# Kernel optimization log

Measured on AMD Instinct MI355X. Metric: run time of the kernel, lower is better.

Reference implementation:

```python
import jax, jax.numpy as jnp
import numpy as np

B, G, P, C = 16, 14, 16, 3          # batch, patch grid (14x14), patch size, channels
D, DI, HM, L = 384, 768, 1536, 12   # embed_dim, d_inner=expand*D, mlp_hidden=4*D, depth


def _ln(x, g, b, eps=1e-5):
    m = x.mean(-1, keepdims=True)
    v = ((x - m) ** 2).mean(-1, keepdims=True)
    return (x - m) * jax.lax.rsqrt(v + eps) * g + b


def _lin_attn(seq, wi, bi, wo, bo, g, b):
    # LinearAttention fallback: gated pointwise MLP (SiLU(z)*sigmoid(gate)) + LN + proj_out
    zg = seq @ wi + bi
    z, gate = jnp.split(zg, 2, axis=-1)
    z = jax.nn.silu(z) * jax.nn.sigmoid(gate)
    return _ln(z, g, b) @ wo + bo


def setup_inputs():
    key = jax.random.key(0)
    ks = jax.random.split(key, 8)
    def w(k, shape, s=0.02):
        return (jax.random.normal(k, shape) * s).astype(jnp.float32)
    return {
        'x': jax.random.normal(ks[0], (B, C, G * P, G * P), jnp.float32),
        'patch_w': w(ks[1], (C * P * P, D)), 'patch_b': jnp.zeros((D,), jnp.float32),
        'pe_g': jnp.ones((D,), jnp.float32), 'pe_b': jnp.zeros((D,), jnp.float32),
        'pos': w(ks[2], (1, G * G, D)),
        'n1_g': jnp.ones((L, D), jnp.float32), 'n1_b': jnp.zeros((L, D), jnp.float32),
        'pi_w': w(ks[3], (L, 4, D, 2 * DI)), 'pi_b': jnp.zeros((L, 4, 2 * DI), jnp.float32),
        'po_w': w(ks[4], (L, 4, DI, D)), 'po_b': jnp.zeros((L, 4, D), jnp.float32),
        'la_g': jnp.ones((L, 4, DI), jnp.float32), 'la_b': jnp.zeros((L, 4, DI), jnp.float32),
        'mg_w': w(ks[5], (L, 4 * D, D)), 'mg_b': jnp.zeros((L, D), jnp.float32),
        'sn_g': jnp.ones((L, D), jnp.float32), 'sn_b': jnp.zeros((L, D), jnp.float32),
        'n2_g': jnp.ones((L, D), jnp.float32), 'n2_b': jnp.zeros((L, D), jnp.float32),
        'm1_w': w(ks[6], (L, D, HM)), 'm1_b': jnp.zeros((L, HM), jnp.float32),
        'm2_w': w(ks[7], (L, HM, D)), 'm2_b': jnp.zeros((L, D), jnp.float32),
        'fin_g': jnp.ones((D,), jnp.float32), 'fin_b': jnp.zeros((D,), jnp.float32),
    }


def reference(x, patch_w, patch_b, pe_g, pe_b, pos, n1_g, n1_b, pi_w, pi_b, po_w, po_b,
              la_g, la_b, mg_w, mg_b, sn_g, sn_b, n2_g, n2_b, m1_w, m1_b, m2_w, m2_b,
              fin_g, fin_b):
    Bsz = x.shape[0]
    # Patch embed: non-overlapping conv == per-patch linear projection
    patches = x.reshape(Bsz, C, G, P, G, P).transpose(0, 2, 4, 1, 3, 5).reshape(Bsz, G, G, C * P * P)
    h = _ln(patches @ patch_w + patch_b, pe_g, pe_b)          # [B, G, G, D]
    h = (h.reshape(Bsz, G * G, D) + pos).reshape(Bsz, G, G, D)  # pos embed (no interp: grid==base)
    for l in range(L):
        hn = _ln(h, n1_g[l], n1_b[l])
        # 4-direction scan sequences (-> <- down up)
        ht = hn.transpose(0, 2, 1, 3)
        seqs = [hn.reshape(Bsz, G * G, D),
                hn[:, ::-1, ::-1].reshape(Bsz, G * G, D),
                ht.reshape(Bsz, G * G, D),
                ht[:, ::-1, ::-1].reshape(Bsz, G * G, D)]
        outs = []
        for i in range(4):
            o = _lin_attn(seqs[i], pi_w[l, i], pi_b[l, i], po_w[l, i], po_b[l, i], la_g[l, i], la_b[l, i])
            if i == 1:
                o = o[:, ::-1]
            elif i == 2:
                o = o.reshape(Bsz, G, G, D).transpose(0, 2, 1, 3).reshape(Bsz, G * G, D)
            elif i == 3:
                o = o[:, ::-1].reshape(Bsz, G, G, D).transpose(0, 2, 1, 3).reshape(Bsz, G * G, D)
            outs.append(o)
        merged = jnp.concatenate(outs, axis=-1) @ mg_w[l] + mg_b[l]
        merged = _ln(merged, sn_g[l], sn_b[l]).reshape(Bsz, G, G, D)
        h = h + merged
        hn2 = _ln(h, n2_g[l], n2_b[l])
        h = h + (jax.nn.gelu(hn2 @ m1_w[l] + m1_b[l], approximate=False) @ m2_w[l] + m2_b[l])
    return _ln(h.reshape(Bsz, G * G, D), fin_g, fin_b)  # dense features [B, N, D]
```

## Files before the change

### kernel.cpp

```cpp
#include <hip/hip_runtime.h>
#include <math.h>

typedef unsigned short u16;
typedef __bf16 bf16x8 __attribute__((ext_vector_type(8)));
typedef float f32x4 __attribute__((ext_vector_type(4)));

#define L_   12
#define NTOK 3136
#define MP   3200

__device__ __forceinline__ float b2f(u16 v){ return __builtin_bit_cast(float, (unsigned)v<<16); }
__device__ __forceinline__ u16 f2b(float f){
    unsigned u = __builtin_bit_cast(unsigned, f);
    u += 0x7fffu + ((u>>16)&1u);
    return (u16)(u>>16);
}
__device__ __forceinline__ float wsum(float v){
    #pragma unroll
    for (int o=32;o;o>>=1) v += __shfl_xor(v,o);
    return v;
}
__device__ __forceinline__ void gl_lds16(const void* g, void* l){
    __builtin_amdgcn_global_load_lds(
        (const __attribute__((address_space(1))) void*)g,
        (__attribute__((address_space(3))) void*)l, 16, 0, 0);
}

__device__ __host__ __forceinline__ int rho16(int c){
    return (c < 768) ? (((c>>4)<<5) + (c&15)) : ((((c-768)>>4)<<5) + 16 + ((c-768)&15));
}

__global__ __launch_bounds__(256) void k_transpose(const float* __restrict__ src,
                                                   u16* __restrict__ dst, int R, int C){
    __shared__ float t[32][33];
    long long base = (long long)blockIdx.z * R * C;
    int c0 = blockIdx.x<<5, r0 = blockIdx.y<<5;
    int tx = threadIdx.x & 31, ty = threadIdx.x >> 5;
    #pragma unroll
    for (int i=0;i<32;i+=8)
        t[ty+i][tx] = src[base + (long long)(r0+ty+i)*C + c0 + tx];
    __syncthreads();
    #pragma unroll
    for (int i=0;i<32;i+=8)
        dst[base + (long long)(c0+ty+i)*R + r0 + tx] = f2b(t[tx][ty+i]);
}

__global__ __launch_bounds__(256) void k_transpose_pi(const float* __restrict__ src,
                                                      u16* __restrict__ dst){
    const int R = 384, C = 1536;
    __shared__ float t[32][33];
    long long base = (long long)blockIdx.z * R * C;
    int c0 = blockIdx.x<<5, r0 = blockIdx.y<<5;
    int tx = threadIdx.x & 31, ty = threadIdx.x >> 5;
    #pragma unroll
    for (int i=0;i<32;i+=8)
        t[ty+i][tx] = src[base + (long long)(r0+ty+i)*C + c0 + tx];
    __syncthreads();
    #pragma unroll
    for (int i=0;i<32;i+=8){
        int c = c0 + ty + i;
        dst[base + (long long)rho16(c)*R + r0 + tx] = f2b(t[tx][ty+i]);
    }
}

__global__ __launch_bounds__(256) void k_bi(const float* __restrict__ pi_b, float* __restrict__ out){
    int idx = blockIdx.x*256 + threadIdx.x;
    if (idx >= 48*1536) return;
    int slab = idx / 1536, c = idx - slab*1536;
    int l = slab >> 2, dir = slab & 3;
    out[(long long)l*6144 + dir*1536 + rho16(c)] = pi_b[idx];
}

__global__ __launch_bounds__(256) void k_cvt_g(const float4* __restrict__ src,
                                               const float* __restrict__ la_g,
                                               ushort4* __restrict__ dst){
    int i = blockIdx.x*256 + threadIdx.x;
    if (i >= 3538944) return;
    int flat = i*4;
    int z = flat / 294912, rem = flat - z*294912;
    int ci = rem / 384;
    float gsc = la_g[(long long)z*768 + ci];
    float4 v = src[i];
    ushort4 o; o.x=f2b(v.x*gsc); o.y=f2b(v.y*gsc); o.z=f2b(v.z*gsc); o.w=f2b(v.w*gsc);
    dst[i] = o;
}

__global__ __launch_bounds__(384) void k_bw(const float* __restrict__ la_b,
                                            const float* __restrict__ po_w,
                                            const float* __restrict__ po_b,
                                            const float* __restrict__ mg_w,
                                            float* __restrict__ bcb){
    __shared__ float t[384];
    int z = blockIdx.x; int l = z>>2, dir = z&3;
    int i = threadIdx.x;
    const float* pw = po_w + (long long)z*294912;
    const float* lb = la_b + (long long)z*768;
    float s = 0.f;
    for (int ci=0; ci<768; ci++) s = fmaf(lb[ci], pw[(long long)ci*384 + i], s);
    t[i] = s + po_b[(long long)z*384 + i];
    __syncthreads();
    const float* mw = mg_w + (long long)l*589824 + (long long)dir*384*384;
    float o = 0.f;
    for (int m=0;m<384;m++) o = fmaf(t[m], mw[(long long)m*384 + i], o);
    bcb[(long long)z*384 + i] = o;
}

__global__ __launch_bounds__(384) void k_gsum(const u16* __restrict__ WcT, float* __restrict__ G){
    int z = blockIdx.x; int l = z>>2, dir = z&3;
    int n = threadIdx.x;
    const u16* p = WcT + (long long)l*1179648 + (long long)n*3072 + dir*768;
    float s = 0.f;
    for (int ci=0; ci<768; ci+=4){
        ushort4 v = *reinterpret_cast<const ushort4*>(p + ci);
        s += b2f(v.x)+b2f(v.y)+b2f(v.z)+b2f(v.w);
    }
    G[(long long)z*384 + n] = s;
}

__global__ __launch_bounds__(256) void k_stats(const u16* __restrict__ gated,
                                               float* __restrict__ st){
    int unit = blockIdx.x*4 + (threadIdx.x>>6);
    int lane = threadIdx.x & 63;
    const u16* p = gated + (long long)(unit>>2)*3072 + (unit&3)*768;
    float s1 = 0.f, s2 = 0.f;
    #pragma unroll
    for (int i=0;i<3;i++){
        ushort4 v = *reinterpret_cast<const ushort4*>(p + i*256 + lane*4);
        const u16* a = (const u16*)&v;
        #pragma unroll
        for (int q=0;q<4;q++){ float f = b2f(a[q]); s1 += f; s2 += f*f; }
    }
    s1 = wsum(s1); s2 = wsum(s2);
    if (lane==0){
        st[(long long)unit*2]   = s1;
        st[(long long)unit*2+1] = s2;
    }
}

__global__ __launch_bounds__(256) void k_patches(const float* __restrict__ x, u16* __restrict__ out){
    int idx = blockIdx.x*256 + threadIdx.x;
    int row = idx / 768, col = idx - row*768;
    float v = 0.f;
    if (row < NTOK){
        int b = row / 196, t = row - b*196;
        int gi = t / 14, gj = t - gi*14;
        int c = col >> 8, rem = col & 255, pi = rem >> 4, pj = rem & 15;
        v = x[((long long)(b*3 + c)*224 + gi*16 + pi)*224 + gj*16 + pj];
    }
    out[idx] = f2b(v);
}

template<int EPI, int BM>
__global__ __launch_bounds__(256) void gemm_tn(
    const u16* __restrict__ A, int lda, long long aSh, long long aSl,
    const u16* __restrict__ Bt, int ldb, long long bSh, long long bSl,
    const float* __restrict__ bias, long long biasSh, int splitBias,
    void* __restrict__ Cbase, int ldc, long long cSh, long long cSl,
    int K, int zshift, const float* __restrict__ aux)
{
    constexpr int NF = (BM==128) ? 4 : 2;
    constexpr int AI = (BM==128) ? 4 : 2;
    int z = blockIdx.z;
    int zh = z >> zshift, zl = z - (zh << zshift);
    const u16* Az  = A  + zh*aSh + zl*aSl;
    const u16* Btz = Bt + zh*bSh + zl*bSl;
    bool addb = bias && (!splitBias || zl == 0);
    long long cOff = zh*cSh + zl*cSl;
    int m0 = blockIdx.y*BM, n0 = blockIdx.x*128;

    __shared__ u16 As[2][BM*64];
    __shared__ u16 Bs[2][8192];

    int tid = threadIdx.x;
    int lane = tid & 63;
    int w = tid >> 6;
    int wrb = (BM==128) ? (w>>1)*64 : 0;
    int wcb = (BM==128) ? (w&1)*64 : w*32;
    int rsub = lane >> 3, csub = lane & 7;
    int scol = ((csub ^ rsub) << 3);
    int kxor = (lane & 7) << 4;

    const u16* ga[AI]; const u16* gb[4]; int loa[AI], lob[4];
    #pragma unroll
    for (int j=0;j<AI;j++){
        int r = j*32 + w*8 + rsub;
        ga[j] = Az + (long long)(m0 + r)*lda + scol;
        loa[j] = (j*32 + w*8)*64;
    }
    #pragma unroll
    for (int j=0;j<4;j++){
        int r = j*32 + w*8 + rsub;
        gb[j] = Btz + (long long)(n0 + r)*ldb + scol;
        lob[j] = (j*32 + w*8)*64;
    }

    f32x4 acc[4][NF];
    #pragma unroll
    for (int m=0;m<4;m++)
        #pragma unroll
        for (int n=0;n<NF;n++) acc[m][n] = (f32x4){0.f,0.f,0.f,0.f};

    int nkt = K >> 6;

    auto stage = [&](int ko, int p){
        #pragma unroll
        for (int j=0;j<AI;j++) gl_lds16(ga[j] + ko, &As[p][loa[j]]);
        #pragma unroll
        for (int j=0;j<4;j++)  gl_lds16(gb[j] + ko, &Bs[p][lob[j]]);
    };

    stage(0, 0);
    stage(64, 1);

    auto step = [&](int kt, int p){
        if (kt == nkt-1)               asm volatile("s_waitcnt vmcnt(0)" ::: "memory");
        else if constexpr (BM==128)    asm volatile("s_waitcnt vmcnt(8)" ::: "memory");
        else                           asm volatile("s_waitcnt vmcnt(6)" ::: "memory");
        __builtin_amdgcn_s_barrier();
        const char* as = (const char*)As[p];
        const char* bs = (const char*)Bs[p];
        bf16x8 af[2][4], bfr[2][NF];
        #pragma unroll
        for (int kk=0; kk<2; ++kk){
            int kb = ((kk*32 + ((lane>>4)<<3))*2) ^ kxor;
            #pragma unroll
            for (int m=0;m<4;m++){
                int r = wrb + m*16 + (lane&15);
                af[kk][m] = *reinterpret_cast<const bf16x8*>(as + r*128 + kb);
            }
            #pragma unroll
            for (int n=0;n<NF;n++){
                int r = wcb + n*16 + (lane&15);
                bfr[kk][n] = *reinterpret_cast<const bf16x8*>(bs + r*128 + kb);
            }
        }
        asm volatile("s_waitcnt lgkmcnt(0)" ::: "memory");
        __builtin_amdgcn_sched_barrier(0);
        __builtin_amdgcn_s_barrier();
        if (kt+2 < nkt) stage((kt+2)<<6, p);
        #pragma unroll
        for (int kk=0; kk<2; ++kk)
            #pragma unroll
            for (int m=0;m<4;m++)
                #pragma unroll
                for (int n=0;n<NF;n++)
                    acc[m][n] = __builtin_amdgcn_mfma_f32_16x16x32_bf16(af[kk][m], bfr[kk][n], acc[m][n], 0,0,0);
    };

    for (int kt=0; kt<nkt; kt+=2){ step(kt, 0); step(kt+1, 1); }

    int rbase = m0 + wrb;
    int nbase = n0 + wcb;
    if (EPI==3){
        int dir = n0/1536;
        #pragma unroll
        for (int np2=0; np2<NF/2; ++np2){
            int ncz = nbase + (np2*2)*16 + (lane&15);
            int pz  = ncz - dir*1536;
            int ci  = ((pz>>5)<<4) + (pz&15);
            float bz = addb ? bias[ncz]      : 0.f;
            float bg = addb ? bias[ncz+16]   : 0.f;
            #pragma unroll
            for (int m=0;m<4;m++){
                #pragma unroll
                for (int r4=0;r4<4;r4++){
                    int row = rbase + m*16 + ((lane>>4)<<2) + r4;
                    float vz = acc[m][np2*2][r4]   + bz;
                    float vg = acc[m][np2*2+1][r4] + bg;
                    float gv = vz / ((1.f+__expf(-vz))*(1.f+__expf(-vg)));
                    ((u16*)Cbase)[(long long)row*3072 + dir*768 + ci] = f2b(gv);
                }
            }
        }
    } else if (EPI==4){
        #pragma unroll
        for (int m=0;m<4;m++){
            #pragma unroll
            for (int r4=0;r4<4;r4++){
                int row = rbase + m*16 + ((lane>>4)<<2) + r4;
                float st1 = aux[((long long)row*4 + zl)*2];
                float st2 = aux[((long long)row*4 + zl)*2 + 1];
                float mu = st1*(1.f/768.f);
                float rs = rsqrtf(st2*(1.f/768.f) - mu*mu + 1e-5f);
                #pragma unroll
                for (int n=0;n<NF;n++){
                    int ncol = nbase + n*16 + (lane&15);
                    ((float*)Cbase)[(long long)row*ldc + ncol + cOff] = acc[m][n][r4]*rs;
                }
            }
        }
    } else {
        #pragma unroll
        for (int m=0;m<4;m++){
            #pragma unroll
            for (int n=0;n<NF;n++){
                int ncol = nbase + n*16 + (lane&15);
                float bv = addb ? bias[zh*biasSh + ncol] : 0.f;
                #pragma unroll
                for (int r4=0;r4<4;r4++){
                    int row = rbase + m*16 + ((lane>>4)<<2) + r4;
                    float v = acc[m][n][r4] + bv;
                    long long idx = (long long)row*ldc + ncol + cOff;
                    if (EPI==0)      ((u16*)Cbase)[idx] = f2b(v);
                    else if (EPI==1){
                        float gl = 0.5f*v*(1.f + erff(v*0.70710678118f));
                        ((u16*)Cbase)[idx] = f2b(gl);
                    }
                    else             ((float*)Cbase)[idx] = v;
                }
            }
        }
    }
}

template<int MODE>
__global__ __launch_bounds__(256) void k_addln(float* __restrict__ h,
        const float* __restrict__ parts, int np,
        const float* __restrict__ g, const float* __restrict__ b, void* __restrict__ out){
    int row = blockIdx.x*4 + (threadIdx.x>>6);
    int lane = threadIdx.x & 63;
    float* hp = h + (long long)row*384;
    float v[6]; float s = 0.f;
    #pragma unroll
    for (int i=0;i<6;i++){
        int c = lane + i*64;
        float t = hp[c];
        for (int p=0;p<np;p++) t += parts[(long long)p*MP*384 + (long long)row*384 + c];
        v[i] = t; s += t;
    }
    if (MODE==0 && np){
        #pragma unroll
        for (int i=0;i<6;i++) hp[lane + i*64] = v[i];
    }
    float mu = wsum(s)*(1.f/384.f);
    float q = 0.f;
    #pragma unroll
    for (int i=0;i<6;i++){ float d = v[i]-mu; q += d*d; }
    float rs = rsqrtf(wsum(q)*(1.f/384.f) + 1e-5f);
    if (MODE==0){
        u16* op = (u16*)out + (long long)row*384;
        #pragma unroll
        for (int i=0;i<6;i++){ int c = lane + i*64; op[c] = f2b((v[i]-mu)*rs*g[c] + b[c]); }
    } else {
        float* op = (float*)out + (long long)row*384;
        #pragma unroll
        for (int i=0;i<6;i++){ int c = lane + i*64; op[c] = (v[i]-mu)*rs*g[c] + b[c]; }
    }
}

__global__ __launch_bounds__(256) void k_pe_ln(const float* __restrict__ parts,
        const float* __restrict__ g, const float* __restrict__ b,
        const float* __restrict__ pos, float* __restrict__ h,
        const float* __restrict__ n1g, const float* __restrict__ n1b,
        u16* __restrict__ hn){
    int row = blockIdx.x*4 + (threadIdx.x>>6);
    int lane = threadIdx.x & 63;
    float v[6]; float s = 0.f;
    #pragma unroll
    for (int i=0;i<6;i++){
        int c = lane + i*64;
        float t = parts[(long long)row*384 + c] + parts[(long long)MP*384 + (long long)row*384 + c];
        v[i] = t; s += t;
    }
    float mu = wsum(s)*(1.f/384.f);
    float q = 0.f;
    #pragma unroll
    for (int i=0;i<6;i++){ float d = v[i]-mu; q += d*d; }
    float rs = rsqrtf(wsum(q)*(1.f/384.f) + 1e-5f);
    int t = row % 196;
    const float* pp = pos + (long long)t*384;
    float* op = h + (long long)row*384;
    float hv[6]; float s2 = 0.f;
    #pragma unroll
    for (int i=0;i<6;i++){
        int c = lane + i*64;
        float nv = (v[i]-mu)*rs*g[c] + b[c] + pp[c];
        op[c] = nv; hv[i] = nv; s2 += nv;
    }
    float mu2 = wsum(s2)*(1.f/384.f);
    float q2 = 0.f;
    #pragma unroll
    for (int i=0;i<6;i++){ float d = hv[i]-mu2; q2 += d*d; }
    float rs2 = rsqrtf(wsum(q2)*(1.f/384.f) + 1e-5f);
    u16* hp = hn + (long long)row*384;
    #pragma unroll
    for (int i=0;i<6;i++){ int c = lane + i*64; hp[c] = f2b((hv[i]-mu2)*rs2*n1g[c] + n1b[c]); }
}

__global__ __launch_bounds__(256) void k_sn_ln(const float* __restrict__ parts,
        const float* __restrict__ bcb, const float* __restrict__ G,
        const float* __restrict__ st, const float* __restrict__ mgb,
        const float* __restrict__ sg, const float* __restrict__ sb,
        float* __restrict__ h,
        const float* __restrict__ n2g, const float* __restrict__ n2b,
        u16* __restrict__ hn2){
    int row = blockIdx.x*4 + (threadIdx.x>>6);
    int lane = threadIdx.x & 63;
    float murs[4];
    #pragma unroll
    for (int z=0;z<4;z++){
        float st1 = st[((long long)row*4 + z)*2];
        float st2 = st[((long long)row*4 + z)*2 + 1];
        float mu = st1*(1.f/768.f);
        float rs = rsqrtf(st2*(1.f/768.f) - mu*mu + 1e-5f);
        murs[z] = mu*rs;
    }
    float v[6]; float s = 0.f;
    #pragma unroll
    for (int i=0;i<6;i++){
        int c = lane + i*64;
        long long o = (long long)row*384 + c;
        float t = mgb[c];
        #pragma unroll
        for (int z=0;z<4;z++) t += bcb[z*384+c] - murs[z]*G[z*384+c];
        #pragma unroll
        for (int p=0;p<4;p++) t += parts[(long long)p*MP*384 + o];
        v[i] = t; s += t;
    }
    float mu = wsum(s)*(1.f/384.f);
    float q = 0.f;
    #pragma unroll
    for (int i=0;i<6;i++){ float d = v[i]-mu; q += d*d; }
    float rs = rsqrtf(wsum(q)*(1.f/384.f) + 1e-5f);
    float* hp = h + (long long)row*384;
    float hv[6]; float s2 = 0.f;
    #pragma unroll
    for (int i=0;i<6;i++){
        int c = lane + i*64;
        float nv = hp[c] + (v[i]-mu)*rs*sg[c] + sb[c];
        hp[c] = nv; hv[i] = nv; s2 += nv;
    }
    float mu2 = wsum(s2)*(1.f/384.f);
    float q2 = 0.f;
    #pragma unroll
    for (int i=0;i<6;i++){ float d = hv[i]-mu2; q2 += d*d; }
    float rs2 = rsqrtf(wsum(q2)*(1.f/384.f) + 1e-5f);
    u16* op = hn2 + (long long)row*384;
    #pragma unroll
    for (int i=0;i<6;i++){ int c = lane + i*64; op[c] = f2b((hv[i]-mu2)*rs2*n2g[c] + n2b[c]); }
}

extern "C" void kernel_launch(void* const* d_in, const int* in_sizes, int n_in,
                              void* d_out, int out_size, void* d_ws, size_t ws_size,
                              hipStream_t stream)
{
    const float* x      = (const float*)d_in[0];
    const float* patch_w= (const float*)d_in[1];
    const float* patch_b= (const float*)d_in[2];
    const float* pe_g   = (const float*)d_in[3];
    const float* pe_b   = (const float*)d_in[4];
    const float* pos    = (const float*)d_in[5];
    const float* n1_g   = (const float*)d_in[6];
    const float* n1_b   = (const float*)d_in[7];
    const float* pi_w   = (const float*)d_in[8];
    const float* pi_b   = (const float*)d_in[9];
    const float* po_w   = (const float*)d_in[10];
    const float* po_b   = (const float*)d_in[11];
    const float* la_g   = (const float*)d_in[12];
    const float* la_b   = (const float*)d_in[13];
    const float* mg_w   = (const float*)d_in[14];
    const float* mg_b   = (const float*)d_in[15];
    const float* sn_g   = (const float*)d_in[16];
    const float* sn_b   = (const float*)d_in[17];
    const float* n2_g   = (const float*)d_in[18];
    const float* n2_b   = (const float*)d_in[19];
    const float* m1_w   = (const float*)d_in[20];
    const float* m1_b   = (const float*)d_in[21];
    const float* m2_w   = (const float*)d_in[22];
    const float* m2_b   = (const float*)d_in[23];
    const float* fin_g  = (const float*)d_in[24];
    const float* fin_b  = (const float*)d_in[25];

    char* wptr = (char*)d_ws;
    auto carve = [&](long long elems, int esz)->void*{
        void* p = (void*)wptr;
        wptr += ((elems*(long long)esz + 255)/256)*256;
        return p;
    };

    u16* wt_pi  = (u16*)carve(28311552, 2);
    u16* wt_mgr = (u16*)carve(7077888, 2);
    u16* wt_m1  = (u16*)carve(7077888, 2);
    u16* wt_m2  = (u16*)carve(7077888, 2);
    u16* wt_pe  = (u16*)carve(294912, 2);
    u16* po_bf  = (u16*)carve(14155776, 2);
    u16* WcT    = (u16*)carve(14155776, 2);
    float* bcb  = (float*)carve(48*384, 4);
    float* Gs   = (float*)carve(48*384, 4);
    float* stats= (float*)carve(MP*8, 4);
    float* pib_i= (float*)carve(12*6144, 4);
    float* h    = (float*)carve((long long)MP*384, 4);
    float* parts= (float*)carve(4LL*MP*384, 4);
    u16* patches= (u16*)carve((long long)MP*768, 2);
    u16* hn     = (u16*)carve((long long)MP*384, 2);
    u16* gated  = (u16*)carve((long long)MP*3072, 2);
    u16* outs   = (u16*)carve((long long)MP*1536, 2);

    dim3 blk(256);

    k_transpose_pi<<<dim3(48,12,48), blk, 0, stream>>>(pi_w, wt_pi);
    k_bi<<<dim3((48*1536+255)/256), blk, 0, stream>>>(pi_b, pib_i);
    k_transpose<<<dim3(12,12,48), blk, 0, stream>>>(mg_w,   wt_mgr, 384, 384);
    k_transpose<<<dim3(48,12,12), blk, 0, stream>>>(m1_w,   wt_m1, 384, 1536);
    k_transpose<<<dim3(12,48,12), blk, 0, stream>>>(m2_w,   wt_m2, 1536, 384);
    k_transpose<<<dim3(12,24,1),  blk, 0, stream>>>(patch_w,wt_pe, 768, 384);
    k_cvt_g<<<dim3(13824), blk, 0, stream>>>((const float4*)po_w, la_g, (ushort4*)po_bf);
    k_bw<<<dim3(48), dim3(384), 0, stream>>>(la_b, po_w, po_b, mg_w, bcb);
    gemm_tn<0,128><<<dim3(6,3,48), blk, 0, stream>>>(
        wt_mgr, 384, 589824LL, 147456LL,
        po_bf,  384, 1179648LL, 294912LL,
        nullptr, 0, 0,
        WcT, 3072, 1179648LL, 768LL, 384, 2, nullptr);
    k_gsum<<<dim3(48), dim3(384), 0, stream>>>(WcT, Gs);

    k_patches<<<dim3(MP*768/256), blk, 0, stream>>>(x, patches);
    gemm_tn<2,64><<<dim3(3,50,2), blk, 0, stream>>>(
        patches, 768, 0, 384,
        wt_pe,   768, 0, 384,
        patch_b, 0, 1,
        parts, 384, 0, (long long)MP*384, 384, 1, nullptr);
    k_pe_ln<<<dim3(MP/4), blk, 0, stream>>>(parts, pe_g, pe_b, pos, h, n1_g, n1_b, hn);

    for (int l=0; l<L_; ++l){
        gemm_tn<3,128><<<dim3(48,25,1), blk, 0, stream>>>(
            hn, 384, 0, 0,
            wt_pi + (long long)l*2359296, 384, 0, 0,
            pib_i + (long long)l*6144, 0, 0,
            gated, 3072, 0, 0, 384, 0, nullptr);
        k_stats<<<dim3(MP), blk, 0, stream>>>(gated, stats);
        gemm_tn<4,64><<<dim3(3,50,4), blk, 0, stream>>>(
            gated, 3072, 0, 768,
            WcT + (long long)l*1179648, 3072, 0, 768,
            nullptr, 0, 0,
            parts, 384, 0, (long long)MP*384, 768, 2, stats);
        k_sn_ln<<<dim3(MP/4), blk, 0, stream>>>(parts,
                                                bcb + (long long)l*1536, Gs + (long long)l*1536,
                                                stats, mg_b + l*384,
                                                sn_g + l*384, sn_b + l*384,
                                                h, n2_g + l*384, n2_b + l*384, hn);
        gemm_tn<1,64><<<dim3(12,50,1), blk, 0, stream>>>(
            hn, 384, 0, 0,
            wt_m1 + (long long)l*589824, 384, 0, 0,
            m1_b + (long long)l*1536, 0, 0,
            outs, 1536, 0, 0, 384, 0, nullptr);
        gemm_tn<2,64><<<dim3(3,50,4), blk, 0, stream>>>(
            outs, 1536, 0, 384,
            wt_m2 + (long long)l*589824, 1536, 0, 384,
            m2_b + l*384, 0, 1,
            parts, 384, 0, (long long)MP*384, 384, 2, nullptr);
        if (l < L_-1)
            k_addln<0><<<dim3(MP/4), blk, 0, stream>>>(h, parts, 4,
                n1_g + (l+1)*384, n1_b + (l+1)*384, hn);
        else
            k_addln<1><<<dim3(NTOK/4), blk, 0, stream>>>(h, parts, 4,
                fin_g, fin_b, (float*)d_out);
    }
}
```

Measured before the change: 1.395 ms.

## Fold LN mean correction into GEMM epilogue, split bias precompute, halve MLP2 split-K

Splits the serial per-slab bias kernel into two chunked kernels that accumulate with atomics, and sums the four direction biases into one vector per layer. The weight row sums come from a new GEMM epilogue instead of a separate pass. The mean*G correction moves into the merge GEMM epilogue, so the LN kernel reads less. The MLP2 GEMM split-K drops from 4 to 2 parts, cutting partial-sum traffic in the add+LN kernel at the cost of fewer blocks. Atomics need a memset and make results order-dependent.

```diff
diff --git a/kernel.cpp b/kernel.cpp
--- a/kernel.cpp
+++ b/kernel.cpp
@@ -85,36 +85,33 @@
     dst[i] = o;
 }
 
-__global__ __launch_bounds__(384) void k_bw(const float* __restrict__ la_b,
-                                            const float* __restrict__ po_w,
-                                            const float* __restrict__ po_b,
-                                            const float* __restrict__ mg_w,
-                                            float* __restrict__ bcb){
-    __shared__ float t[384];
-    int z = blockIdx.x; int l = z>>2, dir = z&3;
+__global__ __launch_bounds__(384) void k_bw1(const float* __restrict__ la_b,
+                                             const float* __restrict__ po_w,
+                                             float* __restrict__ tvec){
+    int z = blockIdx.x, chunk = blockIdx.y;
     int i = threadIdx.x;
     const float* pw = po_w + (long long)z*294912;
     const float* lb = la_b + (long long)z*768;
     float s = 0.f;
-    for (int ci=0; ci<768; ci++) s = fmaf(lb[ci], pw[(long long)ci*384 + i], s);
-    t[i] = s + po_b[(long long)z*384 + i];
-    __syncthreads();
-    const float* mw = mg_w + (long long)l*589824 + (long long)dir*384*384;
-    float o = 0.f;
-    for (int m=0;m<384;m++) o = fmaf(t[m], mw[(long long)m*384 + i], o);
-    bcb[(long long)z*384 + i] = o;
-}
-
-__global__ __launch_bounds__(384) void k_gsum(const u16* __restrict__ WcT, float* __restrict__ G){
-    int z = blockIdx.x; int l = z>>2, dir = z&3;
-    int n = threadIdx.x;
-    const u16* p = WcT + (long long)l*1179648 + (long long)n*3072 + dir*768;
+    int c0 = chunk*128;
+    for (int ci=c0; ci<c0+128; ci++) s = fmaf(lb[ci], pw[(long long)ci*384 + i], s);
+    atomicAdd(tvec + (long long)z*384 + i, s);
+}
+
+__global__ __launch_bounds__(384) void k_bw2(const float* __restrict__ tvec,
+                                             const float* __restrict__ po_b,
+                                             const float* __restrict__ mg_w,
+                                             float* __restrict__ fullb){
+    int z = blockIdx.x, chunk = blockIdx.y;
+    int l = z>>2, dir = z&3;
+    int i = threadIdx.x;
+    const float* mw = mg_w + (long long)l*589824 + (long long)dir*147456;
+    const float* tv = tvec + (long long)z*384;
+    const float* pb = po_b + (long long)z*384;
     float s = 0.f;
-    for (int ci=0; ci<768; ci+=4){
-        ushort4 v = *reinterpret_cast<const ushort4*>(p + ci);
-        s += b2f(v.x)+b2f(v.y)+b2f(v.z)+b2f(v.w);
-    }
-    G[(long long)z*384 + n] = s;
+    int m0 = chunk*64;
+    for (int m=m0; m<m0+64; m++) s = fmaf(tv[m]+pb[m], mw[(long long)m*384 + i], s);
+    atomicAdd(fullb + (long long)l*384 + i, s);
 }
 
 __global__ __launch_bounds__(256) void k_stats(const u16* __restrict__ gated,
@@ -156,7 +153,7 @@
     const u16* __restrict__ Bt, int ldb, long long bSh, long long bSl,
     const float* __restrict__ bias, long long biasSh, int splitBias,
     void* __restrict__ Cbase, int ldc, long long cSh, long long cSl,
-    int K, int zshift, const float* __restrict__ aux)
+    int K, int zshift, const float* __restrict__ aux, float* __restrict__ auxw)
 {
     constexpr int NF = (BM==128) ? 4 : 2;
     constexpr int AI = (BM==128) ? 4 : 2;
@@ -285,8 +282,28 @@
                 #pragma unroll
                 for (int n=0;n<NF;n++){
                     int ncol = nbase + n*16 + (lane&15);
-                    ((float*)Cbase)[(long long)row*ldc + ncol + cOff] = acc[m][n][r4]*rs;
+                    float gsv = bias[(long long)zl*384 + ncol];
+                    ((float*)Cbase)[(long long)row*ldc + ncol + cOff] = (acc[m][n][r4] - mu*gsv)*rs;
                 }
+            }
+        }
+    } else if (EPI==5){
+        #pragma unroll
+        for (int m=0;m<4;m++){
+            #pragma unroll
+            for (int r4=0;r4<4;r4++){
+                int row = rbase + m*16 + ((lane>>4)<<2) + r4;
+                float s = 0.f;
+                #pragma unroll
+                for (int n=0;n<NF;n++){
+                    int ncol = nbase + n*16 + (lane&15);
+                    u16 rv = f2b(acc[m][n][r4]);
+                    ((u16*)Cbase)[(long long)row*ldc + ncol + cOff] = rv;
+                    s += b2f(rv);
+                }
+                #pragma unroll
+                for (int o=1;o<16;o<<=1) s += __shfl_xor(s, o);
+                if ((lane&15)==0) atomicAdd(auxw + (long long)z*384 + row, s);
             }
         }
     } else {
@@ -388,31 +405,19 @@
 }
 
 __global__ __launch_bounds__(256) void k_sn_ln(const float* __restrict__ parts,
-        const float* __restrict__ bcb, const float* __restrict__ G,
-        const float* __restrict__ st, const float* __restrict__ mgb,
+        const float* __restrict__ fullb, const float* __restrict__ mgb,
         const float* __restrict__ sg, const float* __restrict__ sb,
         float* __restrict__ h,
         const float* __restrict__ n2g, const float* __restrict__ n2b,
         u16* __restrict__ hn2){
     int row = blockIdx.x*4 + (threadIdx.x>>6);
     int lane = threadIdx.x & 63;
-    float murs[4];
-    #pragma unroll
-    for (int z=0;z<4;z++){
-        float st1 = st[((long long)row*4 + z)*2];
-        float st2 = st[((long long)row*4 + z)*2 + 1];
-        float mu = st1*(1.f/768.f);
-        float rs = rsqrtf(st2*(1.f/768.f) - mu*mu + 1e-5f);
-        murs[z] = mu*rs;
-    }
     float v[6]; float s = 0.f;
     #pragma unroll
     for (int i=0;i<6;i++){
         int c = lane + i*64;
         long long o = (long long)row*384 + c;
-        float t = mgb[c];
-        #pragma unroll
-        for (int z=0;z<4;z++) t += bcb[z*384+c] - murs[z]*G[z*384+c];
+        float t = mgb[c] + fullb[c];
         #pragma unroll
         for (int p=0;p<4;p++) t += parts[(long long)p*MP*384 + o];
         v[i] = t; s += t;
@@ -485,8 +490,10 @@
     u16* wt_pe  = (u16*)carve(294912, 2);
     u16* po_bf  = (u16*)carve(14155776, 2);
     u16* WcT    = (u16*)carve(14155776, 2);
-    float* bcb  = (float*)carve(48*384, 4);
     float* Gs   = (float*)carve(48*384, 4);
+    float* tvec = (float*)carve(48*384, 4);
+    float* fullb= (float*)carve(12*384, 4);
+    size_t zbytes = (size_t)((char*)(fullb + 12*384) - (char*)Gs);
     float* stats= (float*)carve(MP*8, 4);
     float* pib_i= (float*)carve(12*6144, 4);
     float* h    = (float*)carve((long long)MP*384, 4);
@@ -498,6 +505,7 @@
 
     dim3 blk(256);
 
+    hipMemsetAsync(Gs, 0, zbytes, stream);
     k_transpose_pi<<<dim3(48,12,48), blk, 0, stream>>>(pi_w, wt_pi);
     k_bi<<<dim3((48*1536+255)/256), blk, 0, stream>>>(pi_b, pib_i);
     k_transpose<<<dim3(12,12,48), blk, 0, stream>>>(mg_w,   wt_mgr, 384, 384);
@@ -505,20 +513,20 @@
     k_transpose<<<dim3(12,48,12), blk, 0, stream>>>(m2_w,   wt_m2, 1536, 384);
     k_transpose<<<dim3(12,24,1),  blk, 0, stream>>>(patch_w,wt_pe, 768, 384);
     k_cvt_g<<<dim3(13824), blk, 0, stream>>>((const float4*)po_w, la_g, (ushort4*)po_bf);
-    k_bw<<<dim3(48), dim3(384), 0, stream>>>(la_b, po_w, po_b, mg_w, bcb);
-    gemm_tn<0,128><<<dim3(6,3,48), blk, 0, stream>>>(
+    k_bw1<<<dim3(48,6), dim3(384), 0, stream>>>(la_b, po_w, tvec);
+    k_bw2<<<dim3(48,6), dim3(384), 0, stream>>>(tvec, po_b, mg_w, fullb);
+    gemm_tn<5,128><<<dim3(6,3,48), blk, 0, stream>>>(
         wt_mgr, 384, 589824LL, 147456LL,
         po_bf,  384, 1179648LL, 294912LL,
         nullptr, 0, 0,
-        WcT, 3072, 1179648LL, 768LL, 384, 2, nullptr);
-    k_gsum<<<dim3(48), dim3(384), 0, stream>>>(WcT, Gs);
+        WcT, 3072, 1179648LL, 768LL, 384, 2, nullptr, Gs);
 
     k_patches<<<dim3(MP*768/256), blk, 0, stream>>>(x, patches);
     gemm_tn<2,64><<<dim3(3,50,2), blk, 0, stream>>>(
         patches, 768, 0, 384,
         wt_pe,   768, 0, 384,
         patch_b, 0, 1,
-        parts, 384, 0, (long long)MP*384, 384, 1, nullptr);
+        parts, 384, 0, (long long)MP*384, 384, 1, nullptr, nullptr);
     k_pe_ln<<<dim3(MP/4), blk, 0, stream>>>(parts, pe_g, pe_b, pos, h, n1_g, n1_b, hn);
 
     for (int l=0; l<L_; ++l){
@@ -526,33 +534,32 @@
             hn, 384, 0, 0,
             wt_pi + (long long)l*2359296, 384, 0, 0,
             pib_i + (long long)l*6144, 0, 0,
-            gated, 3072, 0, 0, 384, 0, nullptr);
+            gated, 3072, 0, 0, 384, 0, nullptr, nullptr);
         k_stats<<<dim3(MP), blk, 0, stream>>>(gated, stats);
         gemm_tn<4,64><<<dim3(3,50,4), blk, 0, stream>>>(
             gated, 3072, 0, 768,
             WcT + (long long)l*1179648, 3072, 0, 768,
-            nullptr, 0, 0,
-            parts, 384, 0, (long long)MP*384, 768, 2, stats);
+            Gs + (long long)l*1536, 0, 0,
+            parts, 384, 0, (long long)MP*384, 768, 2, stats, nullptr);
         k_sn_ln<<<dim3(MP/4), blk, 0, stream>>>(parts,
-                                                bcb + (long long)l*1536, Gs + (long long)l*1536,
-                                                stats, mg_b + l*384,
+                                                fullb + (long long)l*384, mg_b + l*384,
                                                 sn_g + l*384, sn_b + l*384,
                                                 h, n2_g + l*384, n2_b + l*384, hn);
         gemm_tn<1,64><<<dim3(12,50,1), blk, 0, stream>>>(
             hn, 384, 0, 0,
             wt_m1 + (long long)l*589824, 384, 0, 0,
             m1_b + (long long)l*1536, 0, 0,
-            outs, 1536, 0, 0, 384, 0, nullptr);
-        gemm_tn<2,64><<<dim3(3,50,4), blk, 0, stream>>>(
-            outs, 1536, 0, 384,
-            wt_m2 + (long long)l*589824, 1536, 0, 384,
+            outs, 1536, 0, 0, 384, 0, nullptr, nullptr);
+        gemm_tn<2,64><<<dim3(3,50,2), blk, 0, stream>>>(
+            outs, 1536, 0, 768,
+            wt_m2 + (long long)l*589824, 1536, 0, 768,
             m2_b + l*384, 0, 1,
-            parts, 384, 0, (long long)MP*384, 384, 2, nullptr);
+            parts, 384, 0, (long long)MP*384, 768, 1, nullptr, nullptr);
         if (l < L_-1)
-            k_addln<0><<<dim3(MP/4), blk, 0, stream>>>(h, parts, 4,
+            k_addln<0><<<dim3(MP/4), blk, 0, stream>>>(h, parts, 2,
                 n1_g + (l+1)*384, n1_b + (l+1)*384, hn);
         else
-            k_addln<1><<<dim3(NTOK/4), blk, 0, stream>>>(h, parts, 4,
+            k_addln<1><<<dim3(NTOK/4), blk, 0, stream>>>(h, parts, 2,
                 fin_g, fin_b, (float*)d_out);
     }
 }
```

Result: faster. 1.321 ms (-5.3%).
